# Kernel tuning notes

Measured on AMD Instinct MI355X. Metric: run time of the kernel, lower is better.

## Reference

```python
import jax, jax.numpy as jnp
import numpy as np

SCALES = (1, 2, 4, 8, 16, 32, 64, 128)
BETA = 0.25   # args.commit_beta
B, C, T = 64, 512, 128
Q, V = 8, 1024
DEPTH, K = 2, 3


def setup_inputs() -> dict:
    key = jax.random.key(0)
    k1, k2, k3, k4 = jax.random.split(key, 4)
    z = jax.random.normal(k1, (B, C, T), dtype=jnp.float32)
    codebooks = jax.random.normal(k2, (Q, V, C), dtype=jnp.float32)
    # small init so stacked ReLU convs stay numerically sane (fan_in = C*K)
    phi_w = jax.random.normal(k3, (Q, DEPTH, C, C, K), dtype=jnp.float32) * (1.0 / np.sqrt(C * K))
    phi_b = jax.random.normal(k4, (Q, DEPTH, C), dtype=jnp.float32) * 0.01
    return {"z": z, "codebooks": codebooks, "phi_w": phi_w, "phi_b": phi_b}


def _conv1d(x, w, b):
    # x: (B,C,T), w: (C_out,C_in,K), 'same' padding (K//2)
    y = jax.lax.conv_general_dilated(x, w, window_strides=(1,), padding=[(K // 2, K // 2)],
                                     dimension_numbers=('NCH', 'OIH', 'NCH'))
    return y + b[None, :, None]


def _phi(x, w_q, b_q):
    # Phi: DEPTH x (Conv1d + ReLU)
    for d in range(DEPTH):
        x = jax.nn.relu(_conv1d(x, w_q[d], b_q[d]))
    return x


def _quantize(xd, cb):
    # xd: (B,C,s) -> nearest codebook entry per timestep. cb: (V,C)
    s = xd.shape[-1]
    flat = xd.transpose(0, 2, 1).reshape(-1, C)                      # (B*s, C)
    d = (jnp.sum(flat * flat, axis=1, keepdims=True)
         - 2.0 * flat @ cb.T + jnp.sum(cb * cb, axis=1))            # (B*s, V)
    idx = jnp.argmin(d, axis=1)                                      # (B*s,)
    emb = cb[idx].reshape(B, s, C).transpose(0, 2, 1)                # (B,C,s)
    # straight-through (EMA codebook: no grad to codebook)
    quant = xd + jax.lax.stop_gradient(emb - xd)
    return quant, idx.reshape(B, s)


def reference(z, codebooks, phi_w, phi_b):
    z = z.astype(jnp.float32)
    z_ng = jax.lax.stop_gradient(z)
    z_q = z_ng
    z_hat = jnp.zeros_like(z_q)
    losses, usages, perps, all_idx = [], [], [], []
    for q, s in enumerate(SCALES):
        # area downsample == window mean (T divisible by s)
        xd = z_q.reshape(B, C, s, T // s).mean(axis=-1)              # (B,C,s)
        quant, idx = _quantize(xd, codebooks[q])
        up = quant if s == T else jax.image.resize(quant, (B, C, T), method='linear')
        z_hat_q = _phi(up, phi_w[q], phi_b[q])
        z_hat = z_hat + z_hat_q
        z_q = z_q - z_hat_q
        counts = jnp.zeros((V,), jnp.float32).at[idx.ravel()].add(1.0)
        usages.append(jnp.mean((counts > 0).astype(jnp.float32)) * 100.0)
        p = counts / (B * s)
        perps.append(jnp.exp(-jnp.sum(p * jnp.log(p + 1e-10))))
        losses.append(BETA * jnp.mean((jax.lax.stop_gradient(z_hat) - z) ** 2)
                      + jnp.mean((z_hat - z_ng) ** 2))
        all_idx.append(idx)
    nQ = float(len(SCALES))
    usage = sum(usages) / nQ
    loss = sum(losses) / nQ
    perp = sum(perps) / nQ
    z_hat_out = jax.lax.stop_gradient(z_hat) - z_ng + z              # straight-through output
    indices = jnp.concatenate([i for i in all_idx], axis=1)          # (B, sum(scales))
    return z_hat_out, usage, loss, perp, indices
```

## Files before the change

kernel.cpp:

```cpp
#include <hip/hip_runtime.h>
#include <math.h>

#define NB 64
#define NC 512
#define NT 128
#define NQ 8
#define NV 1024
#define NBIG 4194304
#define IDX_STRIDE 255

typedef _Float16 half_t;
typedef half_t f16x8 __attribute__((ext_vector_type(8)));
typedef float  f32x4 __attribute__((ext_vector_type(4)));

#define SC_MAIN 0.015625f
#define SC_MID  2.44140625e-4f

#define GLD16(g, l) __builtin_amdgcn_global_load_lds( \
    (const __attribute__((address_space(1))) unsigned int*)(g), \
    (__attribute__((address_space(3))) unsigned int*)(l), 16, 0, 0)

__device__ inline void split64(float v, half_t& h1, half_t& h2) {
    half_t a = (half_t)(v * 64.f);
    float r = v * 64.f - (float)a;
    h1 = a;
    h2 = (half_t)(r * 64.f);
}
__device__ inline void split1(float v, half_t& h1, half_t& h2) {
    half_t a = (half_t)v;
    float r = v - (float)a;
    h1 = a;
    h2 = (half_t)(r * 64.f);
}

__global__ void init_kernel(float* __restrict__ zhat, int* __restrict__ counts,
                            float* __restrict__ accums) {
    int i = blockIdx.x * 256 + threadIdx.x;
    const int stride = 2048 * 256;
    for (; i < NBIG; i += stride) {
        zhat[i] = 0.f;
        if (i < NQ * NV) counts[i] = 0;
        if (i < 16)      accums[i] = 0.f;
    }
}

__global__ void padzero_kernel(half_t* __restrict__ X1, half_t* __restrict__ X2) {
    int b = blockIdx.x;
    int row = blockIdx.y ? 129 : 0;
    int c = threadIdx.x;
    size_t off = ((size_t)b * 130 + row) * NC + c;
    X1[off] = (half_t)0.f; X2[off] = (half_t)0.f;
}

__global__ void cnorm_kernel(const float* __restrict__ cb, float* __restrict__ cnorm) {
    int wid  = (blockIdx.x * 256 + threadIdx.x) >> 6;
    int lane = threadIdx.x & 63;
    if (wid >= NQ * NV) return;
    const float* row = cb + (size_t)wid * NC;
    float s = 0.f;
    #pragma unroll
    for (int e = 0; e < NC / 64; ++e) { float v = row[lane + e * 64]; s = fmaf(v, v, s); }
    #pragma unroll
    for (int m = 32; m >= 1; m >>= 1) s += __shfl_xor(s, m, 64);
    if (lane == 0) cnorm[wid] = s;
}

__global__ void cbprep_kernel(const float* __restrict__ cb, half_t* __restrict__ CbT) {
    int idx = blockIdx.x * 256 + threadIdx.x;
    int e  = idx & 8191;
    int kt = (idx >> 13) & 7;
    int mt = (idx >> 16) & 7;
    int q  = idx >> 19;
    int m = e >> 6, kk = e & 63;
    int ci = kt * 64 + kk;
    int code = mt * 128 + m;
    float v = cb[((size_t)(q * NV + code)) * NC + ci];
    half_t h1, h2;
    split64(v, h1, h2);
    int off = ((m * 128 + kk * 2) ^ ((m & 7) << 4)) >> 1;
    size_t base = ((((size_t)q * 2 + 0) * 8 + mt) * 8 + kt) * 8192 + off;
    CbT[base] = h1;
    CbT[base + (size_t)8 * 8 * 8192] = h2;
}

__global__ __launch_bounds__(256) void downsample_split_kernel(
        const float* __restrict__ z, const float* __restrict__ zhat,
        half_t* __restrict__ Xd1, half_t* __restrict__ Xd2,
        int s, int log2s) {
    __shared__ float D[64 * 129];
    const int tid = threadIdx.x;
    const int b  = blockIdx.x;
    const int c0 = blockIdx.y << 6;
    const size_t gbase = ((size_t)(b * NC + c0)) * NT;
    #pragma unroll
    for (int i = 0; i < 8; ++i) {
        int idx4 = (i * 256 + tid) * 4;
        float4 zv = *(const float4*)(z    + gbase + idx4);
        float4 hv = *(const float4*)(zhat + gbase + idx4);
        int cc = idx4 >> 7, t = idx4 & 127;
        float* dp = D + cc * 129 + t;
        dp[0] = zv.x - hv.x; dp[1] = zv.y - hv.y; dp[2] = zv.z - hv.z; dp[3] = zv.w - hv.w;
    }
    __syncthreads();
    const int w = NT >> log2s;
    const float invw = 1.f / (float)w;
    for (int idx = tid; idx < (s << 6); idx += 256) {
        int cc = idx & 63;
        int j  = idx >> 6;
        const float* row = D + cc * 129 + j * w;
        float sum = 0.f;
        for (int i = 0; i < w; ++i) sum += row[i];
        float xd = sum * invw;
        half_t h1, h2;
        split1(xd, h1, h2);
        size_t o = ((size_t)(b * s + j)) * NC + c0 + cc;
        Xd1[o] = h1;
        Xd2[o] = h2;
    }
}

__global__ __launch_bounds__(256, 2) void quant_mfma_kernel(
        const half_t* __restrict__ CbTq,
        const half_t* __restrict__ Xd1, const half_t* __restrict__ Xd2,
        const float* __restrict__ cnorm,
        float* __restrict__ pval, int* __restrict__ pidx) {
    __shared__ half_t As1[8192];
    __shared__ half_t As2[8192];
    __shared__ half_t Bs1[4096];
    __shared__ half_t Bs2[4096];
    __shared__ float redv[2][2][2][16];
    __shared__ int   redi[2][2][2][16];
    const int tid = threadIdx.x;
    const int w = tid >> 6, l = tid & 63;
    const int wm = w >> 1, wn = w & 1;
    const int lane16 = l & 15, lhi = l >> 4;
    const int nblk = blockIdx.x, mt = blockIdx.y;
    const int r0 = nblk * 64;
    f32x4 accM[4][2] = {}, accm[4][2] = {};
    const half_t* C1b = CbTq + ((size_t)(0 * 8 + mt)) * (8 * 8192);
    const half_t* C2b = CbTq + ((size_t)(1 * 8 + mt)) * (8 * 8192);
    for (int kt = 0; kt < 8; ++kt) {
        const int ci0 = kt << 6;
        __syncthreads();
        const char* c1src = (const char*)(C1b + (size_t)kt * 8192);
        const char* c2src = (const char*)(C2b + (size_t)kt * 8192);
        #pragma unroll
        for (int i = 0; i < 4; ++i) {
            GLD16(c1src + (i * 256 + tid) * 16, (char*)As1 + i * 4096 + w * 1024);
            GLD16(c2src + (i * 256 + tid) * 16, (char*)As2 + i * 4096 + w * 1024);
        }
        #pragma unroll
        for (int i = 0; i < 2; ++i) {
            int c = i * 256 + tid;
            int n = c >> 3, sub = c & 7;
            size_t soff = ((size_t)(r0 + n)) * NC + ci0 + ((sub ^ (n & 7)) << 3);
            GLD16(Xd1 + soff, (char*)Bs1 + i * 4096 + w * 1024);
            GLD16(Xd2 + soff, (char*)Bs2 + i * 4096 + w * 1024);
        }
        __syncthreads();
        #pragma unroll
        for (int kstep = 0; kstep < 2; ++kstep) {
            const int kb = (kstep * 32 + lhi * 8) * 2;
            f16x8 a1[4], a2[4], b1[2], b2[2];
            #pragma unroll
            for (int im = 0; im < 4; ++im) {
                int m = wm * 64 + im * 16 + lane16;
                int off = (m * 128 + kb) ^ ((m & 7) << 4);
                a1[im] = *(const f16x8*)((const char*)As1 + off);
                a2[im] = *(const f16x8*)((const char*)As2 + off);
            }
            #pragma unroll
            for (int in = 0; in < 2; ++in) {
                int n = wn * 32 + in * 16 + lane16;
                int off = (n * 128 + kb) ^ ((n & 7) << 4);
                b1[in] = *(const f16x8*)((const char*)Bs1 + off);
                b2[in] = *(const f16x8*)((const char*)Bs2 + off);
            }
            #pragma unroll
            for (int im = 0; im < 4; ++im)
                #pragma unroll
                for (int in = 0; in < 2; ++in) {
                    accM[im][in] = __builtin_amdgcn_mfma_f32_16x16x32_f16(a1[im], b1[in], accM[im][in], 0, 0, 0);
                    accm[im][in] = __builtin_amdgcn_mfma_f32_16x16x32_f16(a1[im], b2[in], accm[im][in], 0, 0, 0);
                    accm[im][in] = __builtin_amdgcn_mfma_f32_16x16x32_f16(a2[im], b1[in], accm[im][in], 0, 0, 0);
                }
        }
    }
    float bv[2] = {1e30f, 1e30f};
    int   bi[2] = {0, 0};
    #pragma unroll
    for (int im = 0; im < 4; ++im) {
        int mb = mt * 128 + wm * 64 + im * 16 + lhi * 4;
        float4 cn = *(const float4*)(cnorm + mb);
        const float* cnp = (const float*)&cn;
        #pragma unroll
        for (int in = 0; in < 2; ++in) {
            #pragma unroll
            for (int r = 0; r < 4; ++r) {
                float d = cnp[r] - 2.f * (accM[im][in][r] * SC_MAIN + accm[im][in][r] * SC_MID);
                int code = mb + r;
                if (d < bv[in]) { bv[in] = d; bi[in] = code; }
            }
        }
    }
    #pragma unroll
    for (int m = 16; m <= 32; m <<= 1) {
        #pragma unroll
        for (int in = 0; in < 2; ++in) {
            float ov = __shfl_xor(bv[in], m, 64);
            int   oi = __shfl_xor(bi[in], m, 64);
            if (ov < bv[in] || (ov == bv[in] && oi < bi[in])) { bv[in] = ov; bi[in] = oi; }
        }
    }
    if (lhi == 0) {
        #pragma unroll
        for (int in = 0; in < 2; ++in) { redv[wm][wn][in][lane16] = bv[in]; redi[wm][wn][in][lane16] = bi[in]; }
    }
    __syncthreads();
    if (wm == 0 && lhi == 0) {
        #pragma unroll
        for (int in = 0; in < 2; ++in) {
            float v0 = redv[0][wn][in][lane16]; int i0 = redi[0][wn][in][lane16];
            float v1 = redv[1][wn][in][lane16]; int i1 = redi[1][wn][in][lane16];
            if (v1 < v0 || (v1 == v0 && i1 < i0)) { v0 = v1; i0 = i1; }
            int r = r0 + wn * 32 + in * 16 + lane16;
            pval[(size_t)r * 8 + mt] = v0;
            pidx[(size_t)r * 8 + mt] = i0;
        }
    }
}

__global__ void argmin_final_kernel(const float* __restrict__ pval, const int* __restrict__ pidx,
                                    int* __restrict__ idx_int, int* __restrict__ counts,
                                    float* __restrict__ out_idx, int R, int s, int log2s, int offq) {
    int r = blockIdx.x * 256 + threadIdx.x;
    if (r >= R) return;
    float bv = 1e30f; int bi = 0;
    #pragma unroll
    for (int k = 0; k < 8; ++k) {
        float v = pval[(size_t)r * 8 + k];
        int   i = pidx[(size_t)r * 8 + k];
        if (v < bv || (v == bv && i < bi)) { bv = v; bi = i; }
    }
    idx_int[r] = bi;
    atomicAdd(&counts[bi], 1);
    int b = r >> log2s, j = r & (s - 1);
    out_idx[(size_t)b * IDX_STRIDE + offq + j] = (float)bi;
}

__global__ void upsample_split_kernel(const float* __restrict__ cb, const int* __restrict__ idx_int,
                                      half_t* __restrict__ X1, half_t* __restrict__ X2, int s) {
    int b = blockIdx.x, tp = blockIdx.y, c = threadIdx.x;
    size_t off = ((size_t)b * 130 + tp) * NC + c;
    if (tp == 0 || tp == 129) { X1[off] = (half_t)0.f; X2[off] = (half_t)0.f; return; }
    int t = tp - 1;
    float in = (t + 0.5f) * ((float)s * (1.f / 128.f)) - 0.5f;
    float jf = floorf(in);
    float f = in - jf;
    int j0 = (int)jf;
    int i0 = min(max(j0, 0), s - 1);
    int i1 = min(max(j0 + 1, 0), s - 1);
    const int* ib = idx_int + b * s;
    float v0 = cb[(size_t)ib[i0] * NC + c];
    float v1 = cb[(size_t)ib[i1] * NC + c];
    float v = (1.f - f) * v0 + f * v1;
    half_t h1, h2;
    split1(v, h1, h2);
    X1[off] = h1; X2[off] = h2;
}

__global__ void wprep_kernel(const float* __restrict__ W ,
                             half_t* __restrict__ Wt) {
    int d = blockIdx.y;
    const float* Wd = W + (size_t)d * NC * NC * 3;
    half_t* Wtd = Wt + (size_t)d * (2 * 4 * 24 * 8192);
    int idx = blockIdx.x * 256 + threadIdx.x;
    int e  = idx & 8191;
    int rest = idx >> 13;
    int kt = rest % 24;
    int mtl = rest / 24;
    int m = e >> 6, kk = e & 63;
    int k = kt * 64 + kk;
    int ks = k >> 9, ci = k & 511;
    int co = mtl * 128 + m;
    float v = Wd[((size_t)co * NC + ci) * 3 + ks];
    half_t h1, h2;
    split64(v, h1, h2);
    int off = ((m * 128 + kk * 2) ^ ((m & 7) << 4)) >> 1;
    size_t base = ((size_t)mtl * 24 + kt) * 8192 + off;
    Wtd[base] = h1;
    Wtd[base + (size_t)4 * 24 * 8192] = h2;
}

template<int MODE>
__global__ __launch_bounds__(512, 2) void conv_mfma_kernel(
        const half_t* __restrict__ Wt,
        const half_t* __restrict__ X1, const half_t* __restrict__ X2,
        const float* __restrict__ bias,
        half_t* __restrict__ Y1, half_t* __restrict__ Y2,
        float* __restrict__ zhat, const float* __restrict__ z,
        float* __restrict__ lpart) {
    __shared__ half_t A1a[8192], A2a[8192], B1a[8192], B2a[8192];
    __shared__ half_t A1b[8192], A2b[8192], B1b[8192], B2b[8192];
    const int tid = threadIdx.x;
    const int w = tid >> 6;
    const int wm = w >> 2, wn = w & 3;
    const int l = tid & 63, lane16 = l & 15, lhi = l >> 4;
    const int b = blockIdx.x, mt = blockIdx.y;
    f32x4 accM[4][2] = {}, accm[4][2] = {};
    const half_t* W1b = Wt + ((size_t)(0 * 4 + mt)) * (24 * 8192);
    const half_t* W2b = Wt + ((size_t)(1 * 4 + mt)) * (24 * 8192);

    auto stage = [&](half_t* dA1, half_t* dA2, half_t* dB1, half_t* dB2, int kt) {
        const int ks = kt >> 3, ci0 = (kt & 7) << 6;
        const char* s1 = (const char*)(W1b + (size_t)kt * 8192);
        const char* s2 = (const char*)(W2b + (size_t)kt * 8192);
        const int rowb0 = b * 130 + ks;
        #pragma unroll
        for (int i = 0; i < 2; ++i) {
            int doff = i * 8192 + w * 1024;
            GLD16(s1 + (i * 512 + tid) * 16, (char*)dA1 + doff);
            GLD16(s2 + (i * 512 + tid) * 16, (char*)dA2 + doff);
            int c = i * 512 + tid, n = c >> 3, sub = c & 7;
            size_t soff = (size_t)(rowb0 + n) * NC + ci0 + ((sub ^ (n & 7)) << 3);
            GLD16(X1 + soff, (char*)dB1 + doff);
            GLD16(X2 + soff, (char*)dB2 + doff);
        }
    };
    auto compute = [&](const half_t* A1, const half_t* A2, const half_t* B1, const half_t* B2) {
        #pragma unroll
        for (int kstep = 0; kstep < 2; ++kstep) {
            const int kb = kstep * 64 + lhi * 16;
            f16x8 a1[4], a2[4], b1[2], b2[2];
            #pragma unroll
            for (int im = 0; im < 4; ++im) {
                int m = wm * 64 + im * 16 + lane16;
                int off = (m * 128 + kb) ^ ((m & 7) << 4);
                a1[im] = *(const f16x8*)((const char*)A1 + off);
                a2[im] = *(const f16x8*)((const char*)A2 + off);
            }
            #pragma unroll
            for (int in = 0; in < 2; ++in) {
                int n = wn * 32 + in * 16 + lane16;
                int off = (n * 128 + kb) ^ ((n & 7) << 4);
                b1[in] = *(const f16x8*)((const char*)B1 + off);
                b2[in] = *(const f16x8*)((const char*)B2 + off);
            }
            #pragma unroll
            for (int im = 0; im < 4; ++im)
                #pragma unroll
                for (int in = 0; in < 2; ++in) {
                    accM[im][in] = __builtin_amdgcn_mfma_f32_16x16x32_f16(a1[im], b1[in], accM[im][in], 0, 0, 0);
                    accm[im][in] = __builtin_amdgcn_mfma_f32_16x16x32_f16(a1[im], b2[in], accm[im][in], 0, 0, 0);
                    accm[im][in] = __builtin_amdgcn_mfma_f32_16x16x32_f16(a2[im], b1[in], accm[im][in], 0, 0, 0);
                }
        }
    };

    stage(A1a, A2a, B1a, B2a, 0);
    __syncthreads();
    #pragma unroll 1
    for (int k2 = 0; k2 < 12; ++k2) {
        stage(A1b, A2b, B1b, B2b, 2 * k2 + 1);
        compute(A1a, A2a, B1a, B2a);
        __syncthreads();
        if (k2 < 11) stage(A1a, A2a, B1a, B2a, 2 * k2 + 2);
        compute(A1b, A2b, B1b, B2b);
        __syncthreads();
    }

    float lsum = 0.f;
    #pragma unroll
    for (int im = 0; im < 4; ++im) {
        int mb = mt * 128 + wm * 64 + im * 16 + lhi * 4;
        float bs[4];
        #pragma unroll
        for (int r = 0; r < 4; ++r) bs[r] = bias[mb + r];
        #pragma unroll
        for (int in = 0; in < 2; ++in) {
            int t = wn * 32 + in * 16 + lane16;
            if (MODE == 0) {
                half_t h1v[4], h2v[4];
                #pragma unroll
                for (int r = 0; r < 4; ++r) {
                    float y = accM[im][in][r] * SC_MAIN + accm[im][in][r] * SC_MID + bs[r];
                    y = y > 0.f ? y : 0.f;
                    split1(y, h1v[r], h2v[r]);
                }
                size_t rowoff = ((size_t)(b * 130 + 1 + t)) * NC + mb;
                *(ushort4*)(Y1 + rowoff) = *(const ushort4*)h1v;
                *(ushort4*)(Y2 + rowoff) = *(const ushort4*)h2v;
            } else {
                size_t base = ((size_t)b * NC + mb) * NT + t;
                #pragma unroll
                for (int r = 0; r < 4; ++r) {
                    float y = accM[im][in][r] * SC_MAIN + accm[im][in][r] * SC_MID + bs[r];
                    y = y > 0.f ? y : 0.f;
                    size_t oi = base + (size_t)r * NT;
                    float zn = zhat[oi] + y;
                    zhat[oi] = zn;
                    float d = zn - z[oi];
                    lsum = fmaf(d, d, lsum);
                }
            }
        }
    }
    if (MODE == 1) {
        __syncthreads();
        float* red = (float*)A1a;
        red[tid] = lsum;
        __syncthreads();
        for (int st = 256; st >= 1; st >>= 1) {
            if (tid < st) red[tid] += red[tid + st];
            __syncthreads();
        }
        if (tid == 0) lpart[blockIdx.y * 64 + blockIdx.x] = red[0];
    }
}

__global__ void scale_final_kernel(const float* __restrict__ lpart, const int* __restrict__ counts,
                                   float* __restrict__ accums, float invBS) {
    __shared__ float sm[256];
    __shared__ float se[256];
    __shared__ int   su[256];
    int tid = threadIdx.x;
    float ls = lpart[tid];
    int used = 0; float ent = 0.f;
    #pragma unroll
    for (int k = 0; k < 4; ++k) {
        int cv = counts[tid + k * 256];
        if (cv > 0) used++;
        float p = (float)cv * invBS;
        ent = fmaf(p, logf(p + 1e-10f), ent);
    }
    sm[tid] = ls; se[tid] = ent; su[tid] = used;
    __syncthreads();
    for (int st = 128; st >= 1; st >>= 1) {
        if (tid < st) { sm[tid] += sm[tid + st]; se[tid] += se[tid + st]; su[tid] += su[tid + st]; }
        __syncthreads();
    }
    if (tid == 0) {
        float m = sm[0] * (1.f / (float)NBIG);
        accums[1] += 0.25f * m + m;
        accums[0] += ((float)su[0] * (1.f / 1024.f)) * 100.f;
        accums[2] += expf(-se[0]);
    }
}

__global__ void final_write_kernel(const float* __restrict__ accums, float* __restrict__ outscal) {
    int t = threadIdx.x;
    if (t < 3) outscal[t] = accums[t] * 0.125f;
}

extern "C" void kernel_launch(void* const* d_in, const int* in_sizes, int n_in,
                              void* d_out, int out_size, void* d_ws, size_t ws_size,
                              hipStream_t stream) {
    const float* z  = (const float*)d_in[0];
    const float* cb = (const float*)d_in[1];
    const float* pw = (const float*)d_in[2];
    const float* pb = (const float*)d_in[3];

    float* zhat     = (float*)d_out;
    float* out_scal = zhat + NBIG;
    float* out_idx  = zhat + NBIG + 3;

    char* w = (char*)d_ws;
    half_t* Xd1 = (half_t*)w;  w += (size_t)8192 * NC * 2;
    half_t* Xd2 = (half_t*)w;  w += (size_t)8192 * NC * 2;
    half_t* Xa1 = (half_t*)w;  w += (size_t)NB * 130 * NC * 2;
    half_t* Xa2 = (half_t*)w;  w += (size_t)NB * 130 * NC * 2;
    half_t* Xb1 = (half_t*)w;  w += (size_t)NB * 130 * NC * 2;
    half_t* Xb2 = (half_t*)w;  w += (size_t)NB * 130 * NC * 2;
    half_t* Wt  = (half_t*)w;  w += (size_t)2 * 2 * 4 * 24 * 8192 * 2;
    half_t* CbT = (half_t*)w;  w += (size_t)NQ * 2 * 8 * 8 * 8192 * 2;
    float* pval  = (float*)w;  w += (size_t)8192 * 8 * 4;
    int*   pidx  = (int*)w;    w += (size_t)8192 * 8 * 4;
    int*   idx_i = (int*)w;    w += (size_t)16384 * 4;
    int*   counts= (int*)w;    w += (size_t)NQ * NV * 4;
    float* cnorm = (float*)w;  w += (size_t)NQ * NV * 4;
    float* lpart = (float*)w;  w += (size_t)256 * 4;
    float* accums= (float*)w;  w += 256;

    init_kernel<<<2048, 256, 0, stream>>>(zhat, counts, accums);
    padzero_kernel<<<dim3(64, 2), 512, 0, stream>>>(Xb1, Xb2);
    cnorm_kernel<<<(NQ * NV) / 4, 256, 0, stream>>>(cb, cnorm);
    cbprep_kernel<<<16384, 256, 0, stream>>>(cb, CbT);

    const size_t WT_CONV = (size_t)2 * 4 * 24 * 8192;
    int offq = 0;
    for (int q = 0; q < NQ; ++q) {
        int s = 1 << q;
        int R = NB * s;
        const float* cbq = cb + (size_t)q * NV * NC;
        const float* wq  = pw + (size_t)q * 2 * NC * NC * 3;
        const float* bq0 = pb + (size_t)q * 2 * NC;
        const float* bq1 = bq0 + NC;

        downsample_split_kernel<<<dim3(64, 8), 256, 0, stream>>>(z, zhat, Xd1, Xd2, s, q);
        quant_mfma_kernel<<<dim3(R / 64, 8), 256, 0, stream>>>(
            CbT + (size_t)q * 2 * 8 * 8 * 8192, Xd1, Xd2, cnorm + q * NV, pval, pidx);
        argmin_final_kernel<<<(R + 255) / 256, 256, 0, stream>>>(pval, pidx, idx_i,
                                                                 counts + q * NV, out_idx, R, s, q, offq);
        upsample_split_kernel<<<dim3(64, 130), 512, 0, stream>>>(cbq, idx_i, Xa1, Xa2, s);
        wprep_kernel<<<dim3(3072, 2), 256, 0, stream>>>(wq, Wt);
        conv_mfma_kernel<0><<<dim3(64, 4), 512, 0, stream>>>(
            Wt, Xa1, Xa2, bq0, Xb1, Xb2, nullptr, nullptr, nullptr);
        conv_mfma_kernel<1><<<dim3(64, 4), 512, 0, stream>>>(
            Wt + WT_CONV, Xb1, Xb2, bq1, nullptr, nullptr, zhat, z, lpart);
        scale_final_kernel<<<1, 256, 0, stream>>>(lpart, counts + q * NV, accums, 1.f / (float)(NB * s));
        offq += s;
    }
    final_write_kernel<<<1, 64, 0, stream>>>(accums, out_scal);
}
```

Baseline: 1.022 ms.

## Split K across wave groups in conv MFMA kernel with LDS reduction

Reorganizes the 8 waves of the conv GEMM block into two K-halves, each computing a larger 64x64 output sub-tile per wave. This cuts LDS fragment loads per MFMA and raises register-level reuse. Partial sums from the second K-group are reduced through shared memory before the epilogue. Launch bounds drop the 2-blocks-per-CU hint, so the doubled accumulators can use more registers, and s_setprio is raised around the MFMA burst. Occupancy may fall and there is an extra reduction step.

```diff
diff --git a/kernel.cpp b/kernel.cpp
--- a/kernel.cpp
+++ b/kernel.cpp
@@ -293,21 +293,23 @@
 }
 
 template<int MODE>
-__global__ __launch_bounds__(512, 2) void conv_mfma_kernel(
+__global__ __launch_bounds__(512) void conv_mfma_kernel(
         const half_t* __restrict__ Wt,
         const half_t* __restrict__ X1, const half_t* __restrict__ X2,
         const float* __restrict__ bias,
         half_t* __restrict__ Y1, half_t* __restrict__ Y2,
         float* __restrict__ zhat, const float* __restrict__ z,
         float* __restrict__ lpart) {
-    __shared__ half_t A1a[8192], A2a[8192], B1a[8192], B2a[8192];
-    __shared__ half_t A1b[8192], A2b[8192], B1b[8192], B2b[8192];
+    __shared__ __align__(16) half_t A1a[8192], A2a[8192], B1a[8192], B2a[8192];
+    __shared__ __align__(16) half_t A1b[8192], A2b[8192], B1b[8192], B2b[8192];
     const int tid = threadIdx.x;
     const int w = tid >> 6;
-    const int wm = w >> 2, wn = w & 3;
+    const int wk = w >> 2;
+    const int wm = (w >> 1) & 1, wn = w & 1;
+    const int p  = w & 3;
     const int l = tid & 63, lane16 = l & 15, lhi = l >> 4;
     const int b = blockIdx.x, mt = blockIdx.y;
-    f32x4 accM[4][2] = {}, accm[4][2] = {};
+    f32x4 accM[4][4] = {}, accm[4][4] = {};
     const half_t* W1b = Wt + ((size_t)(0 * 4 + mt)) * (24 * 8192);
     const half_t* W2b = Wt + ((size_t)(1 * 4 + mt)) * (24 * 8192);
 
@@ -328,33 +330,32 @@
         }
     };
     auto compute = [&](const half_t* A1, const half_t* A2, const half_t* B1, const half_t* B2) {
-        #pragma unroll
-        for (int kstep = 0; kstep < 2; ++kstep) {
-            const int kb = kstep * 64 + lhi * 16;
-            f16x8 a1[4], a2[4], b1[2], b2[2];
-            #pragma unroll
-            for (int im = 0; im < 4; ++im) {
-                int m = wm * 64 + im * 16 + lane16;
-                int off = (m * 128 + kb) ^ ((m & 7) << 4);
-                a1[im] = *(const f16x8*)((const char*)A1 + off);
-                a2[im] = *(const f16x8*)((const char*)A2 + off);
+        const int kb = wk * 64 + lhi * 16;
+        f16x8 a1[4], a2[4], b1[4], b2[4];
+        #pragma unroll
+        for (int im = 0; im < 4; ++im) {
+            int m = wm * 64 + im * 16 + lane16;
+            int off = (m * 128 + kb) ^ ((m & 7) << 4);
+            a1[im] = *(const f16x8*)((const char*)A1 + off);
+            a2[im] = *(const f16x8*)((const char*)A2 + off);
+        }
+        #pragma unroll
+        for (int in = 0; in < 4; ++in) {
+            int n = wn * 64 + in * 16 + lane16;
+            int off = (n * 128 + kb) ^ ((n & 7) << 4);
+            b1[in] = *(const f16x8*)((const char*)B1 + off);
+            b2[in] = *(const f16x8*)((const char*)B2 + off);
+        }
+        __builtin_amdgcn_s_setprio(1);
+        #pragma unroll
+        for (int im = 0; im < 4; ++im)
+            #pragma unroll
+            for (int in = 0; in < 4; ++in) {
+                accM[im][in] = __builtin_amdgcn_mfma_f32_16x16x32_f16(a1[im], b1[in], accM[im][in], 0, 0, 0);
+                accm[im][in] = __builtin_amdgcn_mfma_f32_16x16x32_f16(a1[im], b2[in], accm[im][in], 0, 0, 0);
+                accm[im][in] = __builtin_amdgcn_mfma_f32_16x16x32_f16(a2[im], b1[in], accm[im][in], 0, 0, 0);
             }
-            #pragma unroll
-            for (int in = 0; in < 2; ++in) {
-                int n = wn * 32 + in * 16 + lane16;
-                int off = (n * 128 + kb) ^ ((n & 7) << 4);
-                b1[in] = *(const f16x8*)((const char*)B1 + off);
-                b2[in] = *(const f16x8*)((const char*)B2 + off);
-            }
-            #pragma unroll
-            for (int im = 0; im < 4; ++im)
-                #pragma unroll
-                for (int in = 0; in < 2; ++in) {
-                    accM[im][in] = __builtin_amdgcn_mfma_f32_16x16x32_f16(a1[im], b1[in], accM[im][in], 0, 0, 0);
-                    accm[im][in] = __builtin_amdgcn_mfma_f32_16x16x32_f16(a1[im], b2[in], accm[im][in], 0, 0, 0);
-                    accm[im][in] = __builtin_amdgcn_mfma_f32_16x16x32_f16(a2[im], b1[in], accm[im][in], 0, 0, 0);
-                }
-        }
+        __builtin_amdgcn_s_setprio(0);
     };
 
     stage(A1a, A2a, B1a, B2a, 0);
@@ -369,38 +370,69 @@
         __syncthreads();
     }
 
+    f32x4 y[4][4];
+    #pragma unroll
+    for (int im = 0; im < 4; ++im)
+        #pragma unroll
+        for (int in = 0; in < 4; ++in)
+            #pragma unroll
+            for (int r = 0; r < 4; ++r)
+                y[im][in][r] = accM[im][in][r] * SC_MAIN + accm[im][in][r] * SC_MID;
+
+    auto store_part = [&](f32x4* arr, int im) {
+        #pragma unroll
+        for (int in = 0; in < 4; ++in) arr[in * 256 + p * 64 + l] = y[im][in];
+    };
+    auto load_part = [&](const f32x4* arr, int im) {
+        #pragma unroll
+        for (int in = 0; in < 4; ++in) {
+            f32x4 t = arr[in * 256 + p * 64 + l];
+            #pragma unroll
+            for (int r = 0; r < 4; ++r) y[im][in][r] += t[r];
+        }
+    };
+    if (wk == 1) {
+        store_part((f32x4*)A1b, 0); store_part((f32x4*)A2b, 1);
+        store_part((f32x4*)B1b, 2); store_part((f32x4*)B2b, 3);
+    }
+    __syncthreads();
+
     float lsum = 0.f;
-    #pragma unroll
-    for (int im = 0; im < 4; ++im) {
-        int mb = mt * 128 + wm * 64 + im * 16 + lhi * 4;
-        float bs[4];
-        #pragma unroll
-        for (int r = 0; r < 4; ++r) bs[r] = bias[mb + r];
-        #pragma unroll
-        for (int in = 0; in < 2; ++in) {
-            int t = wn * 32 + in * 16 + lane16;
-            if (MODE == 0) {
-                half_t h1v[4], h2v[4];
-                #pragma unroll
-                for (int r = 0; r < 4; ++r) {
-                    float y = accM[im][in][r] * SC_MAIN + accm[im][in][r] * SC_MID + bs[r];
-                    y = y > 0.f ? y : 0.f;
-                    split1(y, h1v[r], h2v[r]);
-                }
-                size_t rowoff = ((size_t)(b * 130 + 1 + t)) * NC + mb;
-                *(ushort4*)(Y1 + rowoff) = *(const ushort4*)h1v;
-                *(ushort4*)(Y2 + rowoff) = *(const ushort4*)h2v;
-            } else {
-                size_t base = ((size_t)b * NC + mb) * NT + t;
-                #pragma unroll
-                for (int r = 0; r < 4; ++r) {
-                    float y = accM[im][in][r] * SC_MAIN + accm[im][in][r] * SC_MID + bs[r];
-                    y = y > 0.f ? y : 0.f;
-                    size_t oi = base + (size_t)r * NT;
-                    float zn = zhat[oi] + y;
-                    zhat[oi] = zn;
-                    float d = zn - z[oi];
-                    lsum = fmaf(d, d, lsum);
+    if (wk == 0) {
+        load_part((const f32x4*)A1b, 0); load_part((const f32x4*)A2b, 1);
+        load_part((const f32x4*)B1b, 2); load_part((const f32x4*)B2b, 3);
+        #pragma unroll
+        for (int im = 0; im < 4; ++im) {
+            int mb = mt * 128 + wm * 64 + im * 16 + lhi * 4;
+            float bs[4];
+            #pragma unroll
+            for (int r = 0; r < 4; ++r) bs[r] = bias[mb + r];
+            #pragma unroll
+            for (int in = 0; in < 4; ++in) {
+                int t = wn * 64 + in * 16 + lane16;
+                if (MODE == 0) {
+                    half_t h1v[4], h2v[4];
+                    #pragma unroll
+                    for (int r = 0; r < 4; ++r) {
+                        float yy = y[im][in][r] + bs[r];
+                        yy = yy > 0.f ? yy : 0.f;
+                        split1(yy, h1v[r], h2v[r]);
+                    }
+                    size_t rowoff = ((size_t)(b * 130 + 1 + t)) * NC + mb;
+                    *(ushort4*)(Y1 + rowoff) = *(const ushort4*)h1v;
+                    *(ushort4*)(Y2 + rowoff) = *(const ushort4*)h2v;
+                } else {
+                    size_t base = ((size_t)b * NC + mb) * NT + t;
+                    #pragma unroll
+                    for (int r = 0; r < 4; ++r) {
+                        float yy = y[im][in][r] + bs[r];
+                        yy = yy > 0.f ? yy : 0.f;
+                        size_t oi = base + (size_t)r * NT;
+                        float zn = zhat[oi] + yy;
+                        zhat[oi] = zn;
+                        float d = zn - z[oi];
+                        lsum = fmaf(d, d, lsum);
+                    }
                 }
             }
         }
```

Result: faster. 985.5 us (-3.6%).
